# Performance work log

Hardware: AMD Instinct MI355X
Metric: run time of the kernel (lower is better)

The kernel has to match this reference:

```python
import jax, jax.numpy as jnp
import numpy as np

N, E, R = 100000, 3200000, 9
G, H1, H2, C = 768, 64, 32, 4


def setup_inputs() -> dict:
    key = jax.random.key(0)
    ks = jax.random.split(key, 16)
    s = lambda k, shp, fan: (jax.random.normal(k, shp, jnp.float32) / np.float32(np.sqrt(fan)))
    return {
        'x': jax.random.normal(ks[0], (N, G), jnp.float32),
        'lengths': jax.random.randint(ks[1], (500,), 1, 200),
        'edge_index': jax.random.randint(ks[2], (2, E), 0, N),
        'edge_type': jax.random.randint(ks[3], (E,), 0, R),
        'Wp': s(ks[4], (G, H1), G), 'bp': jnp.zeros((H1,), jnp.float32),
        'W_rel': s(ks[5], (R, H1, H2), H1),
        'W_root': s(ks[6], (H1, H2), H1), 'b_rgcn': jnp.zeros((H2,), jnp.float32),
        'Wq': s(ks[7], (H2, H2), H2), 'bq': jnp.zeros((H2,), jnp.float32),
        'Wk': s(ks[8], (H2, H2), H2), 'bk': jnp.zeros((H2,), jnp.float32),
        'Wv': s(ks[9], (H2, H2), H2), 'bv': jnp.zeros((H2,), jnp.float32),
        'Wskip': s(ks[10], (H2, H2), H2), 'bskip': jnp.zeros((H2,), jnp.float32),
        'Wf': s(ks[11], (H2, C), H2), 'bf': jnp.zeros((C,), jnp.float32),
    }


def reference(x, lengths, edge_index, edge_type, Wp, bp, W_rel, W_root, b_rgcn,
              Wq, bq, Wk, bk, Wv, bv, Wskip, bskip, Wf, bf):
    n = x.shape[0]
    src, dst = edge_index[0], edge_index[1]

    # feature projection: Linear(g_dim -> h1)
    h = x @ Wp + bp                                        # [N, H1]

    # RGCNConv(h1 -> h2), default aggr='mean': per-relation mean over incoming
    # edges, plus root weight and bias.
    msg = jnp.einsum('eh,eho->eo', h[src], W_rel[edge_type])   # [E, H2]
    seg_rd = edge_type * n + dst                               # (relation, dst) segment id
    cnt = jax.ops.segment_sum(jnp.ones((msg.shape[0],), msg.dtype), seg_rd,
                              num_segments=R * n)              # [R*N]
    norm = 1.0 / jnp.maximum(cnt[seg_rd], 1.0)                 # 1/deg_r(dst) per edge
    agg = jax.ops.segment_sum(msg * norm[:, None], dst, num_segments=n)  # [N, H2]
    h = jax.nn.relu(agg + h @ W_root + b_rgcn)

    # TransformerConv(h2 -> h2, heads=1): softmax attention over incoming edges
    q = h @ Wq + bq
    k = h @ Wk + bk
    v = h @ Wv + bv
    scale = 1.0 / np.float32(np.sqrt(H2))
    logits = jnp.sum(q[dst] * k[src], axis=-1) * scale         # [E]
    m = jax.ops.segment_max(logits, dst, num_segments=n)       # per-dst max (stable softmax)
    p = jnp.exp(logits - m[dst])
    denom = jax.ops.segment_sum(p, dst, num_segments=n)
    alpha = p / denom[dst]                                     # [E]
    attn = jax.ops.segment_sum(alpha[:, None] * v[src], dst, num_segments=n)  # [N, H2]
    h = jax.nn.relu(attn + h @ Wskip + bskip)

    # classifier
    return h @ Wf + bf
```

## Files before the change

kernel.cpp:

```cpp
#include <hip/hip_runtime.h>
#include <hip/hip_bf16.h>
#include <math.h>


#define GDIM 768
#define H1D 64
#define H2D 32
#define NREL 9


__global__ void zero_ints(int* __restrict__ p, int count) {
  for (int i = blockIdx.x * blockDim.x + threadIdx.x; i < count;
       i += gridDim.x * blockDim.x)
    p[i] = 0;
}

__global__ void build_wcat(const float* __restrict__ W_rel,
                           const float* __restrict__ W_root,
                           float* __restrict__ Wcat) {
  int i = blockIdx.x * blockDim.x + threadIdx.x;
  if (i >= H1D * 320) return;
  int k = i / 320, m = i % 320;
  float v;
  if (m < NREL * H2D) {
    int r = m >> 5, o = m & 31;
    v = W_rel[(size_t)r * H1D * H2D + k * H2D + o];
  } else {
    v = W_root[k * H2D + (m - NREL * H2D)];
  }
  Wcat[i] = v;
}

__global__ void build_wqkvs(const float* __restrict__ Wq, const float* __restrict__ Wk,
                            const float* __restrict__ Wv, const float* __restrict__ Ws,
                            const float* __restrict__ bq, const float* __restrict__ bk,
                            const float* __restrict__ bv, const float* __restrict__ bs,
                            float* __restrict__ Wqkvs, float* __restrict__ bqkvs) {
  int i = blockIdx.x * blockDim.x + threadIdx.x;
  if (i < H2D * 128) {
    int k = i / 128, c = i % 128;
    int sel = c >> 5, o = c & 31;
    const float* W = (sel == 0) ? Wq : (sel == 1) ? Wk : (sel == 2) ? Wv : Ws;
    Wqkvs[i] = W[k * H2D + o];
  }
  if (i < 128) {
    int sel = i >> 5, o = i & 31;
    const float* b = (sel == 0) ? bq : (sel == 1) ? bk : (sel == 2) ? bv : bs;
    bqkvs[i] = b[o];
  }
}


template <bool BIAS>
__global__ __launch_bounds__(256) void gemm_tile(
    const float* __restrict__ A, const float* __restrict__ B,
    const float* __restrict__ bias, float* __restrict__ C, int M, int K, int N) {
  __shared__ float As[64][17];
  __shared__ float Bs[16][68];
  const int m0 = blockIdx.x * 64;
  const int n0 = blockIdx.y * 64;
  const int tid = threadIdx.x;
  const int tr = tid >> 4, tc = tid & 15;

  float acc[4][4] = {{0.f}};

  for (int kk = 0; kk < K; kk += 16) {
    {
      int ar = tid >> 2;
      int ac = (tid & 3) * 4;
      float4 av = make_float4(0.f, 0.f, 0.f, 0.f);
      if (m0 + ar < M)
        av = *(const float4*)(A + (size_t)(m0 + ar) * K + kk + ac);
      As[ar][ac + 0] = av.x; As[ar][ac + 1] = av.y;
      As[ar][ac + 2] = av.z; As[ar][ac + 3] = av.w;
    }
    {
      int br = tid >> 4;
      int bc = (tid & 15) * 4;
      float4 bv = *(const float4*)(B + (size_t)(kk + br) * N + n0 + bc);
      *(float4*)(&Bs[br][bc]) = bv;
    }
    __syncthreads();
#pragma unroll
    for (int k = 0; k < 16; ++k) {
      float a0 = As[tr * 4 + 0][k];
      float a1 = As[tr * 4 + 1][k];
      float a2 = As[tr * 4 + 2][k];
      float a3 = As[tr * 4 + 3][k];
      float4 b = *(const float4*)(&Bs[k][tc * 4]);
      acc[0][0] += a0 * b.x; acc[0][1] += a0 * b.y; acc[0][2] += a0 * b.z; acc[0][3] += a0 * b.w;
      acc[1][0] += a1 * b.x; acc[1][1] += a1 * b.y; acc[1][2] += a1 * b.z; acc[1][3] += a1 * b.w;
      acc[2][0] += a2 * b.x; acc[2][1] += a2 * b.y; acc[2][2] += a2 * b.z; acc[2][3] += a2 * b.w;
      acc[3][0] += a3 * b.x; acc[3][1] += a3 * b.y; acc[3][2] += a3 * b.z; acc[3][3] += a3 * b.w;
    }
    __syncthreads();
  }

#pragma unroll
  for (int i = 0; i < 4; ++i) {
    int row = m0 + tr * 4 + i;
    if (row < M) {
      int col = n0 + tc * 4;
      float4 v;
      v.x = acc[i][0]; v.y = acc[i][1]; v.z = acc[i][2]; v.w = acc[i][3];
      if (BIAS) {
        v.x += bias[col + 0]; v.y += bias[col + 1];
        v.z += bias[col + 2]; v.w += bias[col + 3];
      }
      *(float4*)(C + (size_t)row * N + col) = v;
    }
  }
}


__global__ void count_edges(const int* __restrict__ ei, const int* __restrict__ et,
                            int* __restrict__ deg, int* __restrict__ cnt_rd,
                            int e, int n) {
  int i = blockIdx.x * blockDim.x + threadIdx.x;
  if (i >= e) return;
  int dst = ei[e + i];
  int t = et[i];
  atomicAdd(&deg[dst], 1);
  atomicAdd(&cnt_rd[t * n + dst], 1);
}

__global__ void invert_counts(int* __restrict__ cnt_rd, int count) {
  for (int i = blockIdx.x * blockDim.x + threadIdx.x; i < count;
       i += gridDim.x * blockDim.x) {
    int c = cnt_rd[i];
    if (c < 1) c = 1;
    float inv = 1.0f / (float)c;
    ((float*)cnt_rd)[i] = inv;
  }
}

__global__ void scan_block_sums(const int* __restrict__ deg, int* __restrict__ partials,
                                int n) {
  int i = blockIdx.x * 256 + threadIdx.x;
  int v = (i < n) ? deg[i] : 0;
#pragma unroll
  for (int off = 32; off > 0; off >>= 1) v += __shfl_down(v, off, 64);
  __shared__ int wsum[4];
  if ((threadIdx.x & 63) == 0) wsum[threadIdx.x >> 6] = v;
  __syncthreads();
  if (threadIdx.x == 0)
    partials[blockIdx.x] = wsum[0] + wsum[1] + wsum[2] + wsum[3];
}

__global__ void scan_partials(const int* __restrict__ partials,
                              int* __restrict__ blockoff, int nb) {
  __shared__ int s[1024];
  int t = threadIdx.x;
  int v = (t < nb) ? partials[t] : 0;
  s[t] = v;
  __syncthreads();
  for (int off = 1; off < 1024; off <<= 1) {
    int add = (t >= off) ? s[t - off] : 0;
    __syncthreads();
    s[t] += add;
    __syncthreads();
  }
  blockoff[t] = s[t] - v;
}

__global__ void scan_final(const int* __restrict__ deg, const int* __restrict__ blockoff,
                           int* __restrict__ rowptr, int* __restrict__ cursor, int n) {
  int i = blockIdx.x * 256 + threadIdx.x;
  int lane = threadIdx.x & 63;
  int v = (i < n) ? deg[i] : 0;
  int incl = v;
#pragma unroll
  for (int off = 1; off < 64; off <<= 1) {
    int u = __shfl_up(incl, off, 64);
    if (lane >= off) incl += u;
  }
  __shared__ int wsum[4];
  if (lane == 63) wsum[threadIdx.x >> 6] = incl;
  __syncthreads();
  int w = threadIdx.x >> 6;
  int woff = 0;
  for (int j = 0; j < w; ++j) woff += wsum[j];
  int excl = incl - v + woff + blockoff[blockIdx.x];
  if (i < n) {
    rowptr[i] = excl;
    cursor[i] = excl;
  }
}

__global__ void scatter_edges(const int* __restrict__ ei, const int* __restrict__ et,
                              int* __restrict__ cursor, unsigned* __restrict__ csr,
                              int e) {
  int i = blockIdx.x * blockDim.x + threadIdx.x;
  if (i >= e) return;
  int src = ei[i];
  int dst = ei[e + i];
  int t = et[i];
  int pos = atomicAdd(&cursor[dst], 1);
  csr[pos] = (unsigned)src | ((unsigned)t << 20);
}


__global__ __launch_bounds__(256) void rgcn_agg(
    const unsigned* __restrict__ csr, const int* __restrict__ rowptr,
    const int* __restrict__ deg, const float* __restrict__ inv_rd,
    const float* __restrict__ hw, const float* __restrict__ b_rgcn,
    float* __restrict__ h2, int n) {
  int wid = (blockIdx.x * 256 + threadIdx.x) >> 6;
  if (wid >= n) return;
  int lane = threadIdx.x & 63;
  int half = lane >> 5, o = lane & 31;
  int dst = wid;
  int start = rowptr[dst];
  int cnt = deg[dst];
  float acc = 0.f;
  for (int i = half; i < cnt; i += 2) {
    unsigned p = csr[start + i];
    int src = p & 0xFFFFF;
    int r = p >> 20;
    float norm = inv_rd[r * n + dst];
    acc += hw[(size_t)src * 320 + r * 32 + o] * norm;
  }
  acc += __shfl_xor(acc, 32, 64);
  float root = hw[(size_t)dst * 320 + NREL * 32 + o] + b_rgcn[o];
  float v = acc + root;
  v = v > 0.f ? v : 0.f;
  if (half == 0) h2[(size_t)dst * 32 + o] = v;
}


__global__ __launch_bounds__(256) void attn_out(
    const unsigned* __restrict__ csr, const int* __restrict__ rowptr,
    const int* __restrict__ deg, const float* __restrict__ qkvs,
    const float* __restrict__ bskip, const float* __restrict__ Wf,
    const float* __restrict__ bf, float* __restrict__ out, int n) {
  int wid = (blockIdx.x * 256 + threadIdx.x) >> 6;
  if (wid >= n) return;
  int lane = threadIdx.x & 63;
  int half = lane >> 5, o = lane & 31;
  int dst = wid;
  const float scale = 0.1767766952966369f;

  float qv = qkvs[(size_t)dst * 128 + o];
  int start = rowptr[dst];
  int cnt = deg[dst];

  float m = -INFINITY, den = 0.f, acc = 0.f;
  for (int i = half; i < cnt; i += 2) {
    unsigned p = csr[start + i];
    int src = p & 0xFFFFF;
    float kv = qkvs[(size_t)src * 128 + 32 + o];
    float vv = qkvs[(size_t)src * 128 + 64 + o];
    float prod = qv * kv;
    prod += __shfl_xor(prod, 1, 64);
    prod += __shfl_xor(prod, 2, 64);
    prod += __shfl_xor(prod, 4, 64);
    prod += __shfl_xor(prod, 8, 64);
    prod += __shfl_xor(prod, 16, 64);
    float logit = prod * scale;
    float nm = fmaxf(m, logit);
    float c = __expf(m - nm);
    float pp = __expf(logit - nm);
    den = den * c + pp;
    acc = acc * c + pp * vv;
    m = nm;
  }
  float mo = __shfl_xor(m, 32, 64);
  float nm = fmaxf(m, mo);
  float c = (m > -INFINITY) ? __expf(m - nm) : 0.f;
  float sden = den * c, sacc = acc * c;
  sden += __shfl_xor(sden, 32, 64);
  sacc += __shfl_xor(sacc, 32, 64);
  float attn = (sden > 0.f) ? (sacc / sden) : 0.f;

  float sv = qkvs[(size_t)dst * 128 + 96 + o] + bskip[o];
  float h3 = attn + sv;
  h3 = h3 > 0.f ? h3 : 0.f;

#pragma unroll
  for (int cidx = 0; cidx < 4; ++cidx) {
    float t = h3 * Wf[o * 4 + cidx];
    t += __shfl_xor(t, 1, 64);
    t += __shfl_xor(t, 2, 64);
    t += __shfl_xor(t, 4, 64);
    t += __shfl_xor(t, 8, 64);
    t += __shfl_xor(t, 16, 64);
    if (lane == 0) out[(size_t)dst * 4 + cidx] = t + bf[cidx];
  }
}


extern "C" void kernel_launch(void* const* d_in, const int* in_sizes, int n_in,
                              void* d_out, int out_size, void* d_ws, size_t ws_size,
                              hipStream_t stream) {
  const float* x      = (const float*)d_in[0];
  const int*   ei     = (const int*)d_in[2];
  const int*   et     = (const int*)d_in[3];
  const float* Wp     = (const float*)d_in[4];
  const float* bp     = (const float*)d_in[5];
  const float* W_rel  = (const float*)d_in[6];
  const float* W_root = (const float*)d_in[7];
  const float* b_rgcn = (const float*)d_in[8];
  const float* Wq     = (const float*)d_in[9];
  const float* bq     = (const float*)d_in[10];
  const float* Wk     = (const float*)d_in[11];
  const float* bk     = (const float*)d_in[12];
  const float* Wv     = (const float*)d_in[13];
  const float* bv     = (const float*)d_in[14];
  const float* Wskip  = (const float*)d_in[15];
  const float* bskip  = (const float*)d_in[16];
  const float* Wf     = (const float*)d_in[17];
  const float* bf     = (const float*)d_in[18];
  float* out = (float*)d_out;

  const int n = in_sizes[0] / GDIM;
  const int e = in_sizes[3];

  float* ws = (float*)d_ws;
  size_t off = 0;
  float* h1    = ws + off; off += (size_t)n * H1D;
  float* hw    = ws + off; off += (size_t)n * 320;
  float* h2    = ws + off; off += (size_t)n * H2D;
  float* qkvs  = ws + off; off += (size_t)n * 128;
  float* Wcat  = ws + off; off += (size_t)H1D * 320;
  float* Wqkvs = ws + off; off += (size_t)H2D * 128;
  float* bqkvs = ws + off; off += 128;
  int* deg     = (int*)(ws + off); off += n;
  int* cnt_rd  = (int*)(ws + off); off += (size_t)NREL * n;
  int* rowptr  = (int*)(ws + off); off += n;
  int* cursor  = (int*)(ws + off); off += n;
  int* partials= (int*)(ws + off); off += 1024;
  int* blockoff= (int*)(ws + off); off += 1024;
  unsigned* csr= (unsigned*)(ws + off); off += e;

  const int nb = (n + 255) / 256;

  zero_ints<<<2048, 256, 0, stream>>>(deg, n + NREL * n);
  build_wcat<<<(H1D * 320 + 255) / 256, 256, 0, stream>>>(W_rel, W_root, Wcat);
  build_wqkvs<<<(H2D * 128 + 255) / 256, 256, 0, stream>>>(
      Wq, Wk, Wv, Wskip, bq, bk, bv, bskip, Wqkvs, bqkvs);
  {
    dim3 g((n + 63) / 64, H1D / 64);
    gemm_tile<true><<<g, 256, 0, stream>>>(x, Wp, bp, h1, n, GDIM, H1D);
  }
  count_edges<<<(e + 255) / 256, 256, 0, stream>>>(ei, et, deg, cnt_rd, e, n);
  invert_counts<<<2048, 256, 0, stream>>>(cnt_rd, NREL * n);
  scan_block_sums<<<nb, 256, 0, stream>>>(deg, partials, n);
  scan_partials<<<1, 1024, 0, stream>>>(partials, blockoff, nb);
  scan_final<<<nb, 256, 0, stream>>>(deg, blockoff, rowptr, cursor, n);
  scatter_edges<<<(e + 255) / 256, 256, 0, stream>>>(ei, et, cursor, csr, e);
  {
    dim3 g((n + 63) / 64, 320 / 64);
    gemm_tile<false><<<g, 256, 0, stream>>>(h1, Wcat, nullptr, hw, n, H1D, 320);
  }
  {
    int blocks = (n * 64 + 255) / 256;
    rgcn_agg<<<blocks, 256, 0, stream>>>(csr, rowptr, deg, (const float*)cnt_rd,
                                         hw, b_rgcn, h2, n);
  }
  {
    dim3 g((n + 63) / 64, 128 / 64);
    gemm_tile<true><<<g, 256, 0, stream>>>(h2, Wqkvs, bqkvs, qkvs, n, H2D, 128);
  }
  {
    int blocks = (n * 64 + 255) / 256;
    attn_out<<<blocks, 256, 0, stream>>>(csr, rowptr, deg, qkvs, bskip, Wf, bf,
                                         out, n);
  }
}
```

Baseline: 1.509 ms.

## Build CSR via two-level dst bucketing and compute per-relation counts in-warp

```diff
diff --git a/kernel.cpp b/kernel.cpp
--- a/kernel.cpp
+++ b/kernel.cpp
@@ -7,6 +7,12 @@
 #define H1D 64
 #define H2D 32
 #define NREL 9
+#define NBK 98
+#define BKT_SHIFT 10
+#define CHUNK 8192
+
+#define SRC_MASK 0x1FFFFu
+#define PAY_MASK 0x1FFFFFu
 
 
 __global__ void zero_ints(int* __restrict__ p, int count) {
@@ -113,24 +119,85 @@
 }
 
 
-__global__ void count_edges(const int* __restrict__ ei, const int* __restrict__ et,
-                            int* __restrict__ deg, int* __restrict__ cnt_rd,
-                            int e, int n) {
-  int i = blockIdx.x * blockDim.x + threadIdx.x;
-  if (i >= e) return;
-  int dst = ei[e + i];
-  int t = et[i];
-  atomicAdd(&deg[dst], 1);
-  atomicAdd(&cnt_rd[t * n + dst], 1);
-}
-
-__global__ void invert_counts(int* __restrict__ cnt_rd, int count) {
-  for (int i = blockIdx.x * blockDim.x + threadIdx.x; i < count;
-       i += gridDim.x * blockDim.x) {
-    int c = cnt_rd[i];
-    if (c < 1) c = 1;
-    float inv = 1.0f / (float)c;
-    ((float*)cnt_rd)[i] = inv;
+__global__ void bucket_count(const int* __restrict__ ei, int* __restrict__ bucketCnt,
+                             int e) {
+  __shared__ int h[NBK];
+  for (int t = threadIdx.x; t < NBK; t += 256) h[t] = 0;
+  __syncthreads();
+  for (int i = blockIdx.x * 256 + threadIdx.x; i < e; i += gridDim.x * 256)
+    atomicAdd(&h[ei[e + i] >> BKT_SHIFT], 1);
+  __syncthreads();
+  for (int t = threadIdx.x; t < NBK; t += 256) atomicAdd(&bucketCnt[t], h[t]);
+}
+
+__global__ void scan_buckets(const int* __restrict__ bucketCnt,
+                             int* __restrict__ bucketBase,
+                             int* __restrict__ bucketCursor) {
+  __shared__ int s[128];
+  int t = threadIdx.x;
+  int v = (t < NBK) ? bucketCnt[t] : 0;
+  s[t] = v;
+  __syncthreads();
+  for (int off = 1; off < 128; off <<= 1) {
+    int add = (t >= off) ? s[t - off] : 0;
+    __syncthreads();
+    s[t] += add;
+    __syncthreads();
+  }
+  if (t < NBK) {
+    int ex = s[t] - v;
+    bucketBase[t] = ex;
+    bucketCursor[t] = ex;
+  }
+}
+
+__global__ __launch_bounds__(256) void bin_scatter(const int* __restrict__ ei,
+                                                   const int* __restrict__ et,
+                                                   int* __restrict__ bucketCursor,
+                                                   unsigned* __restrict__ binned,
+                                                   int e) {
+  __shared__ int h[NBK];
+  __shared__ int rb[NBK];
+  int cb = blockIdx.x * CHUNK;
+  int cnt = min(CHUNK, e - cb);
+  for (int t = threadIdx.x; t < NBK; t += 256) h[t] = 0;
+  __syncthreads();
+  for (int j = threadIdx.x; j < cnt; j += 256)
+    atomicAdd(&h[ei[e + cb + j] >> BKT_SHIFT], 1);
+  __syncthreads();
+  for (int t = threadIdx.x; t < NBK; t += 256)
+    rb[t] = atomicAdd(&bucketCursor[t], h[t]);
+  __syncthreads();
+  for (int t = threadIdx.x; t < NBK; t += 256) h[t] = 0;
+  __syncthreads();
+  for (int j = threadIdx.x; j < cnt; j += 256) {
+    int dst = ei[e + cb + j];
+    int b = dst >> BKT_SHIFT;
+    unsigned rec = ((unsigned)(dst & 1023) << 21) |
+                   ((unsigned)et[cb + j] << 17) | (unsigned)ei[cb + j];
+    int lp = atomicAdd(&h[b], 1);
+    binned[rb[b] + lp] = rec;
+  }
+}
+
+__global__ __launch_bounds__(256) void deg_hist(const unsigned* __restrict__ binned,
+                                                const int* __restrict__ bucketBase,
+                                                const int* __restrict__ bucketCnt,
+                                                int* __restrict__ deg, int n) {
+  __shared__ int d[1024];
+  int bkt = blockIdx.x >> 2, part = blockIdx.x & 3;
+  for (int t = threadIdx.x; t < 1024; t += 256) d[t] = 0;
+  __syncthreads();
+  int base = bucketBase[bkt], bc = bucketCnt[bkt];
+  int q = (bc + 3) >> 2;
+  int s0 = part * q, s1 = min(s0 + q, bc);
+  for (int j = s0 + threadIdx.x; j < s1; j += 256)
+    atomicAdd(&d[binned[base + j] >> 21], 1);
+  __syncthreads();
+  int d0 = bkt << BKT_SHIFT;
+  for (int t = threadIdx.x; t < 1024; t += 256) {
+    int dst = d0 + t;
+    if (dst < n && d[t]) atomicAdd(&deg[dst], d[t]);
   }
 }
 
@@ -187,44 +254,58 @@
   }
 }
 
-__global__ void scatter_edges(const int* __restrict__ ei, const int* __restrict__ et,
-                              int* __restrict__ cursor, unsigned* __restrict__ csr,
-                              int e) {
-  int i = blockIdx.x * blockDim.x + threadIdx.x;
-  if (i >= e) return;
-  int src = ei[i];
-  int dst = ei[e + i];
-  int t = et[i];
-  int pos = atomicAdd(&cursor[dst], 1);
-  csr[pos] = (unsigned)src | ((unsigned)t << 20);
+__global__ __launch_bounds__(256) void csr_scatter(const unsigned* __restrict__ binned,
+                                                   const int* __restrict__ bucketBase,
+                                                   const int* __restrict__ bucketCnt,
+                                                   int* __restrict__ cursor,
+                                                   unsigned* __restrict__ csr, int n) {
+  int bkt = blockIdx.x >> 2, part = blockIdx.x & 3;
+  int base = bucketBase[bkt], bc = bucketCnt[bkt];
+  int q = (bc + 3) >> 2;
+  int s0 = part * q, s1 = min(s0 + q, bc);
+  int d0 = bkt << BKT_SHIFT;
+  for (int j = s0 + threadIdx.x; j < s1; j += 256) {
+    unsigned rec = binned[base + j];
+    int dst = d0 + (int)(rec >> 21);
+    int pos = atomicAdd(&cursor[dst], 1);
+    csr[pos] = rec & PAY_MASK;
+  }
 }
 
 
 __global__ __launch_bounds__(256) void rgcn_agg(
     const unsigned* __restrict__ csr, const int* __restrict__ rowptr,
-    const int* __restrict__ deg, const float* __restrict__ inv_rd,
-    const float* __restrict__ hw, const float* __restrict__ b_rgcn,
-    float* __restrict__ h2, int n) {
+    const int* __restrict__ deg, const float* __restrict__ hw,
+    const float* __restrict__ b_rgcn, float* __restrict__ h2, int n) {
   int wid = (blockIdx.x * 256 + threadIdx.x) >> 6;
   if (wid >= n) return;
   int lane = threadIdx.x & 63;
   int half = lane >> 5, o = lane & 31;
-  int dst = wid;
-  int start = rowptr[dst];
-  int cnt = deg[dst];
+  int start = rowptr[wid];
+  int cnt = deg[wid];
+
+  int rc = 0;
+  for (int i = half; i < cnt; i += 2) {
+    unsigned p = csr[start + i];
+    int r = (p >> 17) & 0xF;
+    rc += (r == o) ? 1 : 0;
+  }
+  rc += __shfl_xor(rc, 32, 64);
+  float inv = 1.0f / (float)max(rc, 1);
+
   float acc = 0.f;
   for (int i = half; i < cnt; i += 2) {
     unsigned p = csr[start + i];
-    int src = p & 0xFFFFF;
-    int r = p >> 20;
-    float norm = inv_rd[r * n + dst];
+    int src = p & SRC_MASK;
+    int r = (p >> 17) & 0xF;
+    float norm = __shfl(inv, r, 32);
     acc += hw[(size_t)src * 320 + r * 32 + o] * norm;
   }
   acc += __shfl_xor(acc, 32, 64);
-  float root = hw[(size_t)dst * 320 + NREL * 32 + o] + b_rgcn[o];
+  float root = hw[(size_t)wid * 320 + NREL * 32 + o] + b_rgcn[o];
   float v = acc + root;
   v = v > 0.f ? v : 0.f;
-  if (half == 0) h2[(size_t)dst * 32 + o] = v;
+  if (half == 0) h2[(size_t)wid * 32 + o] = v;
 }
 
 
@@ -237,17 +318,16 @@
   if (wid >= n) return;
   int lane = threadIdx.x & 63;
   int half = lane >> 5, o = lane & 31;
-  int dst = wid;
   const float scale = 0.1767766952966369f;
 
-  float qv = qkvs[(size_t)dst * 128 + o];
-  int start = rowptr[dst];
-  int cnt = deg[dst];
+  float qv = qkvs[(size_t)wid * 128 + o];
+  int start = rowptr[wid];
+  int cnt = deg[wid];
 
   float m = -INFINITY, den = 0.f, acc = 0.f;
   for (int i = half; i < cnt; i += 2) {
     unsigned p = csr[start + i];
-    int src = p & 0xFFFFF;
+    int src = p & SRC_MASK;
     float kv = qkvs[(size_t)src * 128 + 32 + o];
     float vv = qkvs[(size_t)src * 128 + 64 + o];
     float prod = qv * kv;
@@ -272,7 +352,7 @@
   sacc += __shfl_xor(sacc, 32, 64);
   float attn = (sden > 0.f) ? (sacc / sden) : 0.f;
 
-  float sv = qkvs[(size_t)dst * 128 + 96 + o] + bskip[o];
+  float sv = qkvs[(size_t)wid * 128 + 96 + o] + bskip[o];
   float h3 = attn + sv;
   h3 = h3 > 0.f ? h3 : 0.f;
 
@@ -284,7 +364,7 @@
     t += __shfl_xor(t, 4, 64);
     t += __shfl_xor(t, 8, 64);
     t += __shfl_xor(t, 16, 64);
-    if (lane == 0) out[(size_t)dst * 4 + cidx] = t + bf[cidx];
+    if (lane == 0) out[(size_t)wid * 4 + cidx] = t + bf[cidx];
   }
 }
 
@@ -325,16 +405,20 @@
   float* Wqkvs = ws + off; off += (size_t)H2D * 128;
   float* bqkvs = ws + off; off += 128;
   int* deg     = (int*)(ws + off); off += n;
-  int* cnt_rd  = (int*)(ws + off); off += (size_t)NREL * n;
+  int* bucketCnt    = (int*)(ws + off); off += NBK;
+  int* bucketBase   = (int*)(ws + off); off += NBK;
+  int* bucketCursor = (int*)(ws + off); off += NBK;
   int* rowptr  = (int*)(ws + off); off += n;
   int* cursor  = (int*)(ws + off); off += n;
   int* partials= (int*)(ws + off); off += 1024;
   int* blockoff= (int*)(ws + off); off += 1024;
   unsigned* csr= (unsigned*)(ws + off); off += e;
+  unsigned* binned = (unsigned*)h1;
 
   const int nb = (n + 255) / 256;
-
-  zero_ints<<<2048, 256, 0, stream>>>(deg, n + NREL * n);
+  const int nchunks = (e + CHUNK - 1) / CHUNK;
+
+  zero_ints<<<1024, 256, 0, stream>>>(deg, n + NBK);
   build_wcat<<<(H1D * 320 + 255) / 256, 256, 0, stream>>>(W_rel, W_root, Wcat);
   build_wqkvs<<<(H2D * 128 + 255) / 256, 256, 0, stream>>>(
       Wq, Wk, Wv, Wskip, bq, bk, bv, bskip, Wqkvs, bqkvs);
@@ -342,20 +426,21 @@
     dim3 g((n + 63) / 64, H1D / 64);
     gemm_tile<true><<<g, 256, 0, stream>>>(x, Wp, bp, h1, n, GDIM, H1D);
   }
-  count_edges<<<(e + 255) / 256, 256, 0, stream>>>(ei, et, deg, cnt_rd, e, n);
-  invert_counts<<<2048, 256, 0, stream>>>(cnt_rd, NREL * n);
+  {
+    dim3 g((n + 63) / 64, 320 / 64);
+    gemm_tile<false><<<g, 256, 0, stream>>>(h1, Wcat, nullptr, hw, n, H1D, 320);
+  }
+  bucket_count<<<256, 256, 0, stream>>>(ei, bucketCnt, e);
+  scan_buckets<<<1, 128, 0, stream>>>(bucketCnt, bucketBase, bucketCursor);
+  bin_scatter<<<nchunks, 256, 0, stream>>>(ei, et, bucketCursor, binned, e);
+  deg_hist<<<NBK * 4, 256, 0, stream>>>(binned, bucketBase, bucketCnt, deg, n);
   scan_block_sums<<<nb, 256, 0, stream>>>(deg, partials, n);
   scan_partials<<<1, 1024, 0, stream>>>(partials, blockoff, nb);
   scan_final<<<nb, 256, 0, stream>>>(deg, blockoff, rowptr, cursor, n);
-  scatter_edges<<<(e + 255) / 256, 256, 0, stream>>>(ei, et, cursor, csr, e);
-  {
-    dim3 g((n + 63) / 64, 320 / 64);
-    gemm_tile<false><<<g, 256, 0, stream>>>(h1, Wcat, nullptr, hw, n, H1D, 320);
-  }
+  csr_scatter<<<NBK * 4, 256, 0, stream>>>(binned, bucketBase, bucketCnt, cursor, csr, n);
   {
     int blocks = (n * 64 + 255) / 256;
-    rgcn_agg<<<blocks, 256, 0, stream>>>(csr, rowptr, deg, (const float*)cnt_rd,
-                                         hw, b_rgcn, h2, n);
+    rgcn_agg<<<blocks, 256, 0, stream>>>(csr, rowptr, deg, hw, b_rgcn, h2, n);
   }
   {
     dim3 g((n + 63) / 64, 128 / 64);
```

Result: faster. 1.245 ms (-17.5%).
